# Kernel tuning notes

Hardware: AMD Instinct MI355X
Metric: run time of the kernel (lower is better)

Reference implementation:

```python
import jax, jax.numpy as jnp
import numpy as np

EMBED_DIM = 1024
NUM_HEADS = 16
HEAD_DIM = EMBED_DIM // NUM_HEADS
B, S = 2, 2048


def _xavier(k, shape):
    # xavier_uniform for square [out,in] weight
    limit = float(np.sqrt(6.0 / (shape[0] + shape[1])))
    return jax.random.uniform(k, shape, jnp.float32, -limit, limit)


def setup_inputs() -> dict:
    key = jax.random.key(0)
    ks = jax.random.split(key, 7)
    return {
        "query": jax.random.normal(ks[0], (B, S, EMBED_DIM), jnp.float32),
        "key": jax.random.normal(ks[1], (B, S, EMBED_DIM), jnp.float32),
        "value": jax.random.normal(ks[2], (B, S, EMBED_DIM), jnp.float32),
        "Wq": _xavier(ks[3], (EMBED_DIM, EMBED_DIM)),
        "Wk": _xavier(ks[4], (EMBED_DIM, EMBED_DIM)),
        "Wv": _xavier(ks[5], (EMBED_DIM, EMBED_DIM)),
        "Wo": _xavier(ks[6], (EMBED_DIM, EMBED_DIM)),
    }


def _orthogonalize(Wq, Wk):
    # Both projections computed from the ORIGINAL weights, then both replaced
    # (matches torch: weight1_proj/weight2_proj computed before copy_).
    Wq_o = Wq - Wq @ (Wk.T @ Wk)
    Wk_o = Wk - Wk @ (Wq.T @ Wq)
    return Wq_o, Wk_o


def reference(query, key, value, Wq, Wk, Wv, Wo):
    Wq_o, Wk_o = _orthogonalize(Wq, Wk)
    # F.linear(x, W) = x @ W.T
    q = query @ Wq_o.T
    k = key @ Wk_o.T
    v = value @ Wv.T
    # [B, S, E] -> [B, H, S, Dh]
    def split_heads(x):
        return x.reshape(B, -1, NUM_HEADS, HEAD_DIM).transpose(0, 2, 1, 3)
    q, k, v = split_heads(q), split_heads(k), split_heads(v)
    scale = 1.0 / (HEAD_DIM ** 0.5)
    scores = jnp.einsum("bhqd,bhkd->bhqk", q, k) * scale
    attn = jax.nn.softmax(scores, axis=-1)
    out = jnp.einsum("bhqk,bhkd->bhqd", attn, v)
    out = out.transpose(0, 2, 1, 3).reshape(B, -1, EMBED_DIM)
    return out @ Wo.T
```

## Files before the change

### kernel.cpp

```cpp
#include <hip/hip_runtime.h>
#include <math.h>

constexpr int EMBED  = 1024;
constexpr int NHEADS = 16;
constexpr int HDIM   = 64;
constexpr int BATCH  = 2;
constexpr int SEQ    = 2048;
constexpr int MROWS  = BATCH * SEQ;

typedef unsigned short u16b;
typedef __attribute__((ext_vector_type(8))) short bfrag;
typedef __attribute__((ext_vector_type(4))) float ffrag;

#define SCALE_Q 0.18033688f

__device__ __forceinline__ u16b f2b(float f) {
    union { float f; unsigned u; } v; v.f = f;
    unsigned r = v.u + 0x7fffu + ((v.u >> 16) & 1u);
    return (u16b)(r >> 16);
}
__device__ __forceinline__ u16b f2b_fast(float f) {
    union { float f; unsigned u; } v; v.f = f;
    return (u16b)((v.u + 0x8000u) >> 16);
}

__device__ __forceinline__ void gload_lds16(const u16b* g, u16b* l) {
    __builtin_amdgcn_global_load_lds(
        (const __attribute__((address_space(1))) void*)g,
        (__attribute__((address_space(3))) void*)l,
        16, 0, 0);
}

struct GemmPtrs {
    const u16b* A[3];
    const u16b* B[3];
    const float* D[3];
    u16b* Cb[3];
    float* Cf[3];
    float scale[3];
    int vt[3];
    int hs[3];
};

__global__ void prep_all(const float* __restrict__ q, const float* __restrict__ k,
                         const float* __restrict__ v,
                         const float* __restrict__ Wq, const float* __restrict__ Wk,
                         const float* __restrict__ Wv, const float* __restrict__ Wo,
                         u16b* __restrict__ oq, u16b* __restrict__ ok, u16b* __restrict__ ov,
                         u16b* __restrict__ wq, u16b* __restrict__ wk,
                         u16b* __restrict__ wv, u16b* __restrict__ wo,
                         u16b* __restrict__ wqt, u16b* __restrict__ wkt) {
    const int z = blockIdx.z;
    const int tid = threadIdx.x;
    if (z < 3) {
        const float* src = (z == 0) ? q : (z == 1) ? k : v;
        u16b* dst = (z == 0) ? oq : (z == 1) ? ok : ov;
        const int i = blockIdx.x * 256 + tid;
        float4 val = ((const float4*)src)[i];
        ushort4 o;
        o.x = f2b(val.x); o.y = f2b(val.y); o.z = f2b(val.z); o.w = f2b(val.w);
        ((ushort4*)dst)[i] = o;
        return;
    }
    if (blockIdx.x >= 1024) return;
    const int w = z - 3;
    const float* src = (w == 0) ? Wq : (w == 1) ? Wk : (w == 2) ? Wv : Wo;
    u16b* dst  = (w == 0) ? wq : (w == 1) ? wk : (w == 2) ? wv : wo;
    u16b* dstT = (w == 0) ? wqt : (w == 1) ? wkt : nullptr;
    __shared__ float t[32][33];
    const int bx = (blockIdx.x & 31) * 32, by = (blockIdx.x >> 5) * 32;
    const int x = tid & 31, y = tid >> 5;
#pragma unroll
    for (int r = 0; r < 4; ++r) {
        const int row = by + y + 8 * r;
        const float val = src[(size_t)row * EMBED + bx + x];
        dst[(size_t)row * EMBED + bx + x] = f2b(val);
        if (w < 2) t[y + 8 * r][x] = val;
    }
    if (w >= 2) return;
    __syncthreads();
#pragma unroll
    for (int r = 0; r < 4; ++r)
        dstT[(size_t)(bx + y + 8 * r) * EMBED + by + x] = f2b(t[x][y + 8 * r]);
}

template<int MODE>
__global__ __launch_bounds__(256) void gemm64(GemmPtrs p, int M, int N, int K) {
    const int z = blockIdx.z;
    const u16b* __restrict__ A = p.A[z];
    const u16b* __restrict__ B = p.B[z];
    const float* __restrict__ D = p.D[z];
    u16b* __restrict__ Cb = p.Cb[z];
    const float scale = p.scale[z];

    __shared__ __align__(16) u16b As[64 * 32];
    __shared__ __align__(16) u16b Bs[64 * 32];

    const int tid = threadIdx.x;
    const int wave = tid >> 6, lane = tid & 63;
    const int quad = lane >> 4, l16 = lane & 15;
    const int wrow = wave >> 1, wcol = wave & 1;
    const int m0 = blockIdx.y * 64, n0 = blockIdx.x * 64;

    ffrag acc[2][2];
#pragma unroll
    for (int i = 0; i < 2; ++i)
#pragma unroll
        for (int j = 0; j < 2; ++j) acc[i][j] = ffrag{0.f, 0.f, 0.f, 0.f};

    const int srow = tid >> 2, schunk = tid & 3;

    for (int kt = 0; kt < K; kt += 32) {
        gload_lds16(A + (size_t)(m0 + srow) * K + kt + schunk * 8, &As[wave * 512]);
        gload_lds16(B + (size_t)(n0 + srow) * K + kt + schunk * 8, &Bs[wave * 512]);
        __syncthreads();
        bfrag a[2], bv[2];
#pragma unroll
        for (int i = 0; i < 2; ++i)
            a[i] = *(const bfrag*)&As[(wrow * 32 + i * 16 + l16) * 32 + quad * 8];
#pragma unroll
        for (int j = 0; j < 2; ++j)
            bv[j] = *(const bfrag*)&Bs[(wcol * 32 + j * 16 + l16) * 32 + quad * 8];
#pragma unroll
        for (int i = 0; i < 2; ++i)
#pragma unroll
            for (int j = 0; j < 2; ++j)
                acc[i][j] = __builtin_amdgcn_mfma_f32_16x16x32_bf16(a[i], bv[j], acc[i][j], 0, 0, 0);
        __syncthreads();
    }

#pragma unroll
    for (int i = 0; i < 2; ++i)
#pragma unroll
        for (int j = 0; j < 2; ++j) {
            const int col = n0 + wcol * 32 + j * 16 + l16;
#pragma unroll
            for (int r = 0; r < 4; ++r) {
                const int row = m0 + wrow * 32 + i * 16 + quad * 4 + r;
                const size_t idx = (size_t)row * N + col;
                const float v = acc[i][j][r];
                if (MODE == 0) Cb[idx] = f2b(v * scale);
                else Cb[idx] = f2b(D[idx] - v);
            }
        }
}

template<int MODE, int BM>
__global__ __launch_bounds__(256) void gemm_big(GemmPtrs p, int M, int N, int K) {
    const int z = blockIdx.z;
    const u16b* __restrict__ A = p.A[z];
    const u16b* __restrict__ B = p.B[z];
    u16b* __restrict__ Cb = p.Cb[z];
    float* __restrict__ Cf = p.Cf[z];
    const float scale = p.scale[z];
    const int vt = p.vt[z], hs = p.hs[z];

    constexpr int BK = 32;
    constexpr int IT = BM / 32;
    constexpr int IA = BM / 64;
    __shared__ __align__(16) u16b As[BM * BK];
    __shared__ __align__(16) u16b Bs[128 * BK];

    const int tid = threadIdx.x;
    const int wave = tid >> 6, lane = tid & 63;
    const int quad = lane >> 4, l16 = lane & 15;
    const int wrow = wave >> 1, wcol = wave & 1;
    const int m0 = blockIdx.y * BM, n0 = blockIdx.x * 128;

    ffrag acc[IT][4];
#pragma unroll
    for (int i = 0; i < IT; ++i)
#pragma unroll
        for (int j = 0; j < 4; ++j) acc[i][j] = ffrag{0.f, 0.f, 0.f, 0.f};

    const int srow = lane >> 2, schunk = lane & 3;

    for (int kt = 0; kt < K; kt += BK) {
#pragma unroll
        for (int q = 0; q < IA; ++q) {
            int row = wave * (BM / 4) + q * 16;
            gload_lds16(A + (size_t)(m0 + row + srow) * K + kt + schunk * 8, &As[row * BK]);
        }
#pragma unroll
        for (int q = 0; q < 2; ++q) {
            int row = wave * 32 + q * 16;
            gload_lds16(B + (size_t)(n0 + row + srow) * K + kt + schunk * 8, &Bs[row * BK]);
        }
        __syncthreads();
        bfrag af[IT], bfv[4];
#pragma unroll
        for (int i = 0; i < IT; ++i)
            af[i] = *(const bfrag*)&As[(wrow * (BM / 2) + i * 16 + l16) * BK + quad * 8];
#pragma unroll
        for (int j = 0; j < 4; ++j)
            bfv[j] = *(const bfrag*)&Bs[(wcol * 64 + j * 16 + l16) * BK + quad * 8];
#pragma unroll
        for (int i = 0; i < IT; ++i)
#pragma unroll
            for (int j = 0; j < 4; ++j)
                acc[i][j] = __builtin_amdgcn_mfma_f32_16x16x32_bf16(af[i], bfv[j], acc[i][j], 0, 0, 0);
        __syncthreads();
    }

    if (MODE == 0 && vt) {
#pragma unroll
        for (int i = 0; i < IT; ++i)
#pragma unroll
            for (int j = 0; j < 4; ++j) {
                const int col = n0 + wcol * 64 + j * 16 + l16;
                const int h = col >> 6, d = col & 63;
                const int row0 = m0 + wrow * (BM / 2) + i * 16 + quad * 4;
                const int b = row0 >> 11, s = row0 & 2047;
                ushort4 o;
                o.x = f2b(acc[i][j][0]); o.y = f2b(acc[i][j][1]);
                o.z = f2b(acc[i][j][2]); o.w = f2b(acc[i][j][3]);
                *(ushort4*)&Cb[((size_t)(b * NHEADS + h) * HDIM + d) * SEQ + s] = o;
            }
        return;
    }
    if (MODE == 0 && hs) {
#pragma unroll
        for (int i = 0; i < IT; ++i)
#pragma unroll
            for (int j = 0; j < 4; ++j) {
                const int col = n0 + wcol * 64 + j * 16 + l16;
                const int h = col >> 6, d = col & 63;
                const int row0 = m0 + wrow * (BM / 2) + i * 16 + quad * 4;
                const int b = row0 >> 11, s0 = row0 & 2047;
#pragma unroll
                for (int r = 0; r < 4; ++r)
                    Cb[((size_t)(b * NHEADS + h) * SEQ + s0 + r) * HDIM + d] =
                        f2b(acc[i][j][r] * scale);
            }
        return;
    }

#pragma unroll
    for (int i = 0; i < IT; ++i)
#pragma unroll
        for (int j = 0; j < 4; ++j) {
            const int col = n0 + wcol * 64 + j * 16 + l16;
#pragma unroll
            for (int r = 0; r < 4; ++r) {
                const int row = m0 + wrow * (BM / 2) + i * 16 + quad * 4 + r;
                const size_t idx = (size_t)row * N + col;
                const float v = acc[i][j][r];
                if (MODE == 0) Cb[idx] = f2b(v * scale);
                else Cf[idx] = v;
            }
        }
}

__global__ __launch_bounds__(256) void flash_attn5(
    const u16b* __restrict__ Qp, const u16b* __restrict__ Kp,
    const u16b* __restrict__ Vt, float* __restrict__ Opart,
    float* __restrict__ Lpart)
{
    const int tid = threadIdx.x;
    const int wave = tid >> 6, lane = tid & 63;
    const int quad = lane >> 4, l16 = lane & 15;
    const int qt = blockIdx.x, h = blockIdx.y;
    const int b = blockIdx.z >> 1, sp = blockIdx.z & 1;
    const int qb = qt * 128 + wave * 32;
    const int kt0 = sp * (SEQ / 2), kt1 = kt0 + SEQ / 2;

    __shared__ __align__(16) u16b Ks[2][64 * 64];
    __shared__ __align__(16) u16b Vs[2][64 * 64];
    __shared__ __align__(16) u16b Ps[4][2][16][72];

    const size_t hsbase = (size_t)(b * NHEADS + h) * SEQ;
    const size_t vtbase = (size_t)(b * NHEADS + h) * HDIM * SEQ;
    const size_t obase  = ((size_t)sp * MROWS + (size_t)b * SEQ) * EMBED + h * HDIM;

    bfrag bq[2][2];
#pragma unroll
    for (int u = 0; u < 2; ++u)
#pragma unroll
        for (int s = 0; s < 2; ++s)
            bq[u][s] = *(const bfrag*)&Qp[(hsbase + qb + u * 16 + l16) * HDIM + s * 32 + quad * 8];

    ffrag ov[2][4];
#pragma unroll
    for (int u = 0; u < 2; ++u)
#pragma unroll
        for (int t = 0; t < 4; ++t) ov[u][t] = ffrag{0.f, 0.f, 0.f, 0.f};
    float l_run[2] = {0.f, 0.f};

    const int r0 = tid >> 3, c0 = tid & 7;
    const int sw0 = (r0 * 8 + (c0 ^ (r0 & 7))) * 8;
    const int sw1 = ((r0 + 32) * 8 + (c0 ^ (r0 & 7))) * 8;
    const u16b* kgb = Kp + hsbase * HDIM;
    const u16b* vgb = Vt + vtbase;

    {
        const u16b* kg = kgb + (size_t)kt0 * HDIM;
        bfrag k0 = *(const bfrag*)(kg + tid * 8);
        bfrag k1 = *(const bfrag*)(kg + (tid + 256) * 8);
        bfrag v0 = *(const bfrag*)(vgb + (size_t)r0 * SEQ + kt0 + c0 * 8);
        bfrag v1 = *(const bfrag*)(vgb + (size_t)(r0 + 32) * SEQ + kt0 + c0 * 8);
        *(bfrag*)&Ks[0][sw0] = k0;  *(bfrag*)&Ks[0][sw1] = k1;
        *(bfrag*)&Vs[0][sw0] = v0;  *(bfrag*)&Vs[0][sw1] = v1;
    }
    __syncthreads();

    int p = 0;
    for (int kt = kt0; kt < kt1; kt += 64, p ^= 1) {
        const bool more = (kt + 64) < kt1;
        bfrag kn0, kn1, vn0, vn1;
        if (more) {
            const u16b* kg = kgb + (size_t)(kt + 64) * HDIM;
            kn0 = *(const bfrag*)(kg + tid * 8);
            kn1 = *(const bfrag*)(kg + (tid + 256) * 8);
            vn0 = *(const bfrag*)(vgb + (size_t)r0 * SEQ + kt + 64 + c0 * 8);
            vn1 = *(const bfrag*)(vgb + (size_t)(r0 + 32) * SEQ + kt + 64 + c0 * 8);
        }

        ffrag St[2][4];
#pragma unroll
        for (int u = 0; u < 2; ++u)
#pragma unroll
            for (int t = 0; t < 4; ++t) St[u][t] = ffrag{0.f, 0.f, 0.f, 0.f};
#pragma unroll
        for (int t = 0; t < 4; ++t) {
            const int row = t * 16 + l16;
#pragma unroll
            for (int s = 0; s < 2; ++s) {
                const int ch = quad + s * 4;
                bfrag kf = *(const bfrag*)&Ks[p][(row * 8 + (ch ^ (row & 7))) * 8];
#pragma unroll
                for (int u = 0; u < 2; ++u)
                    St[u][t] = __builtin_amdgcn_mfma_f32_16x16x32_bf16(kf, bq[u][s], St[u][t], 0, 0, 0);
            }
        }

#pragma unroll
        for (int u = 0; u < 2; ++u) {
            float rs = 0.f;
#pragma unroll
            for (int t = 0; t < 4; ++t)
#pragma unroll
                for (int r = 0; r < 4; ++r) {
                    const float pv = __builtin_amdgcn_exp2f(St[u][t][r]);
                    St[u][t][r] = pv;
                    rs += pv;
                }
            rs += __shfl_xor(rs, 16);
            rs += __shfl_xor(rs, 32);
            l_run[u] += rs;
        }

#pragma unroll
        for (int u = 0; u < 2; ++u)
#pragma unroll
            for (int t = 0; t < 4; ++t) {
                ushort4 pk;
                pk.x = f2b_fast(St[u][t][0]); pk.y = f2b_fast(St[u][t][1]);
                pk.z = f2b_fast(St[u][t][2]); pk.w = f2b_fast(St[u][t][3]);
                *(ushort4*)&Ps[wave][u][l16][t * 16 + quad * 4] = pk;
            }
        asm volatile("s_waitcnt lgkmcnt(0)" ::: "memory");
        bfrag bp[2][2];
#pragma unroll
        for (int u = 0; u < 2; ++u)
#pragma unroll
            for (int s = 0; s < 2; ++s)
                bp[u][s] = *(const bfrag*)&Ps[wave][u][l16][s * 32 + quad * 8];

#pragma unroll
        for (int t = 0; t < 4; ++t) {
            const int row = t * 16 + l16;
#pragma unroll
            for (int s = 0; s < 2; ++s) {
                const int ch = quad + s * 4;
                bfrag vf = *(const bfrag*)&Vs[p][(row * 8 + (ch ^ (row & 7))) * 8];
#pragma unroll
                for (int u = 0; u < 2; ++u)
                    ov[u][t] = __builtin_amdgcn_mfma_f32_16x16x32_bf16(vf, bp[u][s], ov[u][t], 0, 0, 0);
            }
        }

        if (more) {
            *(bfrag*)&Ks[p ^ 1][sw0] = kn0;  *(bfrag*)&Ks[p ^ 1][sw1] = kn1;
            *(bfrag*)&Vs[p ^ 1][sw0] = vn0;  *(bfrag*)&Vs[p ^ 1][sw1] = vn1;
            __syncthreads();
        }
    }

#pragma unroll
    for (int u = 0; u < 2; ++u) {
#pragma unroll
        for (int t = 0; t < 4; ++t) {
            float4 o;
            o.x = ov[u][t][0]; o.y = ov[u][t][1];
            o.z = ov[u][t][2]; o.w = ov[u][t][3];
            *(float4*)&Opart[obase + (size_t)(qb + u * 16 + l16) * EMBED + t * 16 + quad * 4] = o;
        }
        if (quad == 0)
            Lpart[((size_t)sp * BATCH * NHEADS + b * NHEADS + h) * SEQ + qb + u * 16 + l16] = l_run[u];
    }
}

__global__ void combine_o(const float* __restrict__ O0, const float* __restrict__ O1,
                          const float* __restrict__ L0, const float* __restrict__ L1,
                          u16b* __restrict__ ao) {
    const int i = blockIdx.x * 256 + threadIdx.x;
    const int e0 = i << 2;
    const int row = e0 >> 10, col = e0 & 1023;
    const int lidx = ((row >> 11) * NHEADS + (col >> 6)) * SEQ + (row & 2047);
    float4 a = ((const float4*)O0)[i];
    float4 c = ((const float4*)O1)[i];
    const float inv = 1.f / (L0[lidx] + L1[lidx]);
    ushort4 o;
    o.x = f2b((a.x + c.x) * inv); o.y = f2b((a.y + c.y) * inv);
    o.z = f2b((a.z + c.z) * inv); o.w = f2b((a.w + c.w) * inv);
    ((ushort4*)ao)[i] = o;
}

extern "C" void kernel_launch(void* const* d_in, const int* in_sizes, int n_in,
                              void* d_out, int out_size, void* d_ws, size_t ws_size,
                              hipStream_t stream) {
    const float* query = (const float*)d_in[0];
    const float* key_  = (const float*)d_in[1];
    const float* value = (const float*)d_in[2];
    const float* Wq    = (const float*)d_in[3];
    const float* Wk    = (const float*)d_in[4];
    const float* Wv    = (const float*)d_in[5];
    const float* Wo    = (const float*)d_in[6];
    float* out = (float*)d_out;

    char* ws = (char*)d_ws;
    const size_t MB = 1024 * 1024;
    u16b* xq  = (u16b*)(ws + 0 * MB);
    u16b* xk  = (u16b*)(ws + 8 * MB);
    u16b* xv  = (u16b*)(ws + 16 * MB);
    u16b* wq  = (u16b*)(ws + 24 * MB);
    u16b* wk  = (u16b*)(ws + 26 * MB);
    u16b* wv  = (u16b*)(ws + 28 * MB);
    u16b* gq  = (u16b*)(ws + 32 * MB);
    u16b* gk  = (u16b*)(ws + 34 * MB);
    u16b* wqo = (u16b*)(ws + 36 * MB);
    u16b* wko = (u16b*)(ws + 38 * MB);
    u16b* wo  = (u16b*)(ws + 40 * MB);
    u16b* qp  = (u16b*)(ws + 44 * MB);
    u16b* kp  = (u16b*)(ws + 52 * MB);
    u16b* Vt  = (u16b*)(ws + 60 * MB);
    u16b* wqt = (u16b*)(ws + 60 * MB);
    u16b* wkt = (u16b*)(ws + 62 * MB);
    float* Op  = (float*)(ws + 0 * MB);
    float* Lp  = (float*)(ws + 32 * MB);
    u16b*  ao  = (u16b*)(ws + 44 * MB);

    prep_all<<<dim3(MROWS * EMBED / 1024, 1, 7), dim3(256), 0, stream>>>(
        query, key_, value, Wq, Wk, Wv, Wo,
        xq, xk, xv, wq, wk, wv, wo, wqt, wkt);

    {
        GemmPtrs p{};
        p.A[0] = wqt; p.B[0] = wqt; p.Cb[0] = gq; p.scale[0] = 1.f;
        p.A[1] = wkt; p.B[1] = wkt; p.Cb[1] = gk; p.scale[1] = 1.f;
        gemm64<0><<<dim3(16, 16, 2), dim3(256), 0, stream>>>(p, EMBED, EMBED, EMBED);
    }
    {
        GemmPtrs p{};
        p.A[0] = wq; p.B[0] = gk; p.D[0] = Wq; p.Cb[0] = wqo;
        p.A[1] = wk; p.B[1] = gq; p.D[1] = Wk; p.Cb[1] = wko;
        gemm64<1><<<dim3(16, 16, 2), dim3(256), 0, stream>>>(p, EMBED, EMBED, EMBED);
    }
    {
        GemmPtrs p{};
        p.A[0] = xq; p.B[0] = wqo; p.Cb[0] = qp; p.scale[0] = SCALE_Q; p.hs[0] = 1;
        p.A[1] = xk; p.B[1] = wko; p.Cb[1] = kp; p.scale[1] = 1.f;     p.hs[1] = 1;
        p.A[2] = xv; p.B[2] = wv;  p.Cb[2] = Vt; p.scale[2] = 1.f;     p.vt[2] = 1;
        gemm_big<0, 128><<<dim3(EMBED / 128, MROWS / 128, 3), dim3(256), 0, stream>>>(
            p, MROWS, EMBED, EMBED);
    }
    flash_attn5<<<dim3(SEQ / 128, NHEADS, BATCH * 2), dim3(256), 0, stream>>>(
        qp, kp, Vt, Op, Lp);
    combine_o<<<dim3(MROWS * EMBED / 1024), dim3(256), 0, stream>>>(
        Op, Op + (size_t)MROWS * EMBED, Lp, Lp + (size_t)BATCH * NHEADS * SEQ, ao);
    {
        GemmPtrs p{};
        p.A[0] = ao; p.B[0] = wo; p.Cf[0] = out; p.scale[0] = 1.f;
        gemm_big<2, 64><<<dim3(EMBED / 128, MROWS / 64, 1), dim3(256), 0, stream>>>(
            p, MROWS, EMBED, EMBED);
    }
}
```

Measured before the change: 294.9 us.

## Use 32x32x16 MFMA in attention and keep P in registers via permlane swaps

Result: no change. 293.3 us (-0.5%).

```diff
diff --git a/kernel.cpp b/kernel.cpp
--- a/kernel.cpp
+++ b/kernel.cpp
@@ -11,6 +11,8 @@
 typedef unsigned short u16b;
 typedef __attribute__((ext_vector_type(8))) short bfrag;
 typedef __attribute__((ext_vector_type(4))) float ffrag;
+typedef __attribute__((ext_vector_type(16))) float f16frag;
+typedef __attribute__((ext_vector_type(4))) int i32x4;
 
 #define SCALE_Q 0.18033688f
 
@@ -19,9 +21,17 @@
     unsigned r = v.u + 0x7fffu + ((v.u >> 16) & 1u);
     return (u16b)(r >> 16);
 }
-__device__ __forceinline__ u16b f2b_fast(float f) {
-    union { float f; unsigned u; } v; v.f = f;
-    return (u16b)((v.u + 0x8000u) >> 16);
+
+__device__ __forceinline__ unsigned cvtpk_bf16(float a, float b) {
+    unsigned r;
+    asm("v_cvt_pk_bf16_f32 %0, %1, %2" : "=v"(r) : "v"(a), "v"(b));
+    return r;
+}
+
+__device__ __forceinline__ void plane_swap(unsigned a, unsigned b, int& lo, int& hi) {
+    auto r = __builtin_amdgcn_permlane32_swap((int)a, (int)b, false, false);
+    lo = (int)r[0];
+    hi = (int)r[1];
 }
 
 __device__ __forceinline__ void gload_lds16(const u16b* g, u16b* l) {
@@ -251,14 +261,14 @@
         }
 }
 
-__global__ __launch_bounds__(256) void flash_attn5(
+__global__ __launch_bounds__(256) void flash_attn6(
     const u16b* __restrict__ Qp, const u16b* __restrict__ Kp,
     const u16b* __restrict__ Vt, float* __restrict__ Opart,
     float* __restrict__ Lpart)
 {
     const int tid = threadIdx.x;
     const int wave = tid >> 6, lane = tid & 63;
-    const int quad = lane >> 4, l16 = lane & 15;
+    const int l32 = lane & 31, hi = lane >> 5;
     const int qt = blockIdx.x, h = blockIdx.y;
     const int b = blockIdx.z >> 1, sp = blockIdx.z & 1;
     const int qb = qt * 128 + wave * 32;
@@ -266,25 +276,20 @@
 
     __shared__ __align__(16) u16b Ks[2][64 * 64];
     __shared__ __align__(16) u16b Vs[2][64 * 64];
-    __shared__ __align__(16) u16b Ps[4][2][16][72];
 
     const size_t hsbase = (size_t)(b * NHEADS + h) * SEQ;
     const size_t vtbase = (size_t)(b * NHEADS + h) * HDIM * SEQ;
     const size_t obase  = ((size_t)sp * MROWS + (size_t)b * SEQ) * EMBED + h * HDIM;
 
-    bfrag bq[2][2];
-#pragma unroll
-    for (int u = 0; u < 2; ++u)
-#pragma unroll
-        for (int s = 0; s < 2; ++s)
-            bq[u][s] = *(const bfrag*)&Qp[(hsbase + qb + u * 16 + l16) * HDIM + s * 32 + quad * 8];
-
-    ffrag ov[2][4];
-#pragma unroll
-    for (int u = 0; u < 2; ++u)
-#pragma unroll
-        for (int t = 0; t < 4; ++t) ov[u][t] = ffrag{0.f, 0.f, 0.f, 0.f};
-    float l_run[2] = {0.f, 0.f};
+    bfrag bq[4];
+#pragma unroll
+    for (int ks = 0; ks < 4; ++ks)
+        bq[ks] = *(const bfrag*)&Qp[(hsbase + qb + l32) * HDIM + ks * 16 + hi * 8];
+
+    f16frag ov0, ov1;
+#pragma unroll
+    for (int r = 0; r < 16; ++r) { ov0[r] = 0.f; ov1[r] = 0.f; }
+    float l_run = 0.f;
 
     const int r0 = tid >> 3, c0 = tid & 7;
     const int sw0 = (r0 * 8 + (c0 ^ (r0 & 7))) * 8;
@@ -315,68 +320,66 @@
             vn1 = *(const bfrag*)(vgb + (size_t)(r0 + 32) * SEQ + kt + 64 + c0 * 8);
         }
 
-        ffrag St[2][4];
-#pragma unroll
-        for (int u = 0; u < 2; ++u)
-#pragma unroll
-            for (int t = 0; t < 4; ++t) St[u][t] = ffrag{0.f, 0.f, 0.f, 0.f};
-#pragma unroll
-        for (int t = 0; t < 4; ++t) {
-            const int row = t * 16 + l16;
-#pragma unroll
-            for (int s = 0; s < 2; ++s) {
-                const int ch = quad + s * 4;
-                bfrag kf = *(const bfrag*)&Ks[p][(row * 8 + (ch ^ (row & 7))) * 8];
-#pragma unroll
-                for (int u = 0; u < 2; ++u)
-                    St[u][t] = __builtin_amdgcn_mfma_f32_16x16x32_bf16(kf, bq[u][s], St[u][t], 0, 0, 0);
-            }
-        }
-
-#pragma unroll
-        for (int u = 0; u < 2; ++u) {
-            float rs = 0.f;
-#pragma unroll
-            for (int t = 0; t < 4; ++t)
-#pragma unroll
-                for (int r = 0; r < 4; ++r) {
-                    const float pv = __builtin_amdgcn_exp2f(St[u][t][r]);
-                    St[u][t][r] = pv;
-                    rs += pv;
-                }
-            rs += __shfl_xor(rs, 16);
-            rs += __shfl_xor(rs, 32);
-            l_run[u] += rs;
-        }
-
-#pragma unroll
-        for (int u = 0; u < 2; ++u)
-#pragma unroll
-            for (int t = 0; t < 4; ++t) {
-                ushort4 pk;
-                pk.x = f2b_fast(St[u][t][0]); pk.y = f2b_fast(St[u][t][1]);
-                pk.z = f2b_fast(St[u][t][2]); pk.w = f2b_fast(St[u][t][3]);
-                *(ushort4*)&Ps[wave][u][l16][t * 16 + quad * 4] = pk;
-            }
-        asm volatile("s_waitcnt lgkmcnt(0)" ::: "memory");
-        bfrag bp[2][2];
-#pragma unroll
-        for (int u = 0; u < 2; ++u)
-#pragma unroll
-            for (int s = 0; s < 2; ++s)
-                bp[u][s] = *(const bfrag*)&Ps[wave][u][l16][s * 32 + quad * 8];
-
-#pragma unroll
-        for (int t = 0; t < 4; ++t) {
-            const int row = t * 16 + l16;
-#pragma unroll
-            for (int s = 0; s < 2; ++s) {
-                const int ch = quad + s * 4;
-                bfrag vf = *(const bfrag*)&Vs[p][(row * 8 + (ch ^ (row & 7))) * 8];
-#pragma unroll
-                for (int u = 0; u < 2; ++u)
-                    ov[u][t] = __builtin_amdgcn_mfma_f32_16x16x32_bf16(vf, bp[u][s], ov[u][t], 0, 0, 0);
-            }
+        f16frag St0, St1;
+#pragma unroll
+        for (int r = 0; r < 16; ++r) { St0[r] = 0.f; St1[r] = 0.f; }
+#pragma unroll
+        for (int ks = 0; ks < 4; ++ks) {
+            const int ch = ks * 2 + hi;
+            bfrag k0 = *(const bfrag*)&Ks[p][(l32 * 8 + (ch ^ (l32 & 7))) * 8];
+            bfrag k1 = *(const bfrag*)&Ks[p][((32 + l32) * 8 + (ch ^ (l32 & 7))) * 8];
+            St0 = __builtin_amdgcn_mfma_f32_32x32x16_bf16(k0, bq[ks], St0, 0, 0, 0);
+            St1 = __builtin_amdgcn_mfma_f32_32x32x16_bf16(k1, bq[ks], St1, 0, 0, 0);
+        }
+
+        float rs = 0.f;
+#pragma unroll
+        for (int r = 0; r < 16; ++r) {
+            const float a = __builtin_amdgcn_exp2f(St0[r]);
+            const float c = __builtin_amdgcn_exp2f(St1[r]);
+            St0[r] = a; St1[r] = c;
+            rs += a + c;
+        }
+        rs += __shfl_xor(rs, 32);
+        l_run += rs;
+
+        unsigned d0[8], d1[8];
+#pragma unroll
+        for (int rr = 0; rr < 8; ++rr) {
+            d0[rr] = cvtpk_bf16(St0[2 * rr], St0[2 * rr + 1]);
+            d1[rr] = cvtpk_bf16(St1[2 * rr], St1[2 * rr + 1]);
+        }
+        bfrag bp[4];
+        {
+            int a0, a1, b0, b1, c0w, c1, e0, e1;
+            plane_swap(d0[0], d0[2], a0, a1);
+            plane_swap(d0[1], d0[3], b0, b1);
+            i32x4 w = { a0, b0, a1, b1 };
+            bp[0] = __builtin_bit_cast(bfrag, w);
+            plane_swap(d0[4], d0[6], c0w, c1);
+            plane_swap(d0[5], d0[7], e0, e1);
+            i32x4 w2 = { c0w, e0, c1, e1 };
+            bp[1] = __builtin_bit_cast(bfrag, w2);
+        }
+        {
+            int a0, a1, b0, b1, c0w, c1, e0, e1;
+            plane_swap(d1[0], d1[2], a0, a1);
+            plane_swap(d1[1], d1[3], b0, b1);
+            i32x4 w = { a0, b0, a1, b1 };
+            bp[2] = __builtin_bit_cast(bfrag, w);
+            plane_swap(d1[4], d1[6], c0w, c1);
+            plane_swap(d1[5], d1[7], e0, e1);
+            i32x4 w2 = { c0w, e0, c1, e1 };
+            bp[3] = __builtin_bit_cast(bfrag, w2);
+        }
+
+#pragma unroll
+        for (int ks = 0; ks < 4; ++ks) {
+            const int ch = ks * 2 + hi;
+            bfrag v0 = *(const bfrag*)&Vs[p][(l32 * 8 + (ch ^ (l32 & 7))) * 8];
+            bfrag v1 = *(const bfrag*)&Vs[p][((32 + l32) * 8 + (ch ^ (l32 & 7))) * 8];
+            ov0 = __builtin_amdgcn_mfma_f32_32x32x16_bf16(v0, bp[ks], ov0, 0, 0, 0);
+            ov1 = __builtin_amdgcn_mfma_f32_32x32x16_bf16(v1, bp[ks], ov1, 0, 0, 0);
         }
 
         if (more) {
@@ -386,18 +389,19 @@
         }
     }
 
-#pragma unroll
-    for (int u = 0; u < 2; ++u) {
-#pragma unroll
-        for (int t = 0; t < 4; ++t) {
-            float4 o;
-            o.x = ov[u][t][0]; o.y = ov[u][t][1];
-            o.z = ov[u][t][2]; o.w = ov[u][t][3];
-            *(float4*)&Opart[obase + (size_t)(qb + u * 16 + l16) * EMBED + t * 16 + quad * 4] = o;
-        }
-        if (quad == 0)
-            Lpart[((size_t)sp * BATCH * NHEADS + b * NHEADS + h) * SEQ + qb + u * 16 + l16] = l_run[u];
-    }
+    const size_t orow = obase + (size_t)(qb + l32) * EMBED;
+#pragma unroll
+    for (int rr = 0; rr < 4; ++rr) {
+        float4 o0, o1;
+        o0.x = ov0[4 * rr + 0]; o0.y = ov0[4 * rr + 1];
+        o0.z = ov0[4 * rr + 2]; o0.w = ov0[4 * rr + 3];
+        o1.x = ov1[4 * rr + 0]; o1.y = ov1[4 * rr + 1];
+        o1.z = ov1[4 * rr + 2]; o1.w = ov1[4 * rr + 3];
+        *(float4*)&Opart[orow + rr * 8 + hi * 4] = o0;
+        *(float4*)&Opart[orow + 32 + rr * 8 + hi * 4] = o1;
+    }
+    if (hi == 0)
+        Lpart[((size_t)sp * BATCH * NHEADS + b * NHEADS + h) * SEQ + qb + l32] = l_run;
 }
 
 __global__ void combine_o(const float* __restrict__ O0, const float* __restrict__ O1,
@@ -474,7 +478,7 @@
         gemm_big<0, 128><<<dim3(EMBED / 128, MROWS / 128, 3), dim3(256), 0, stream>>>(
             p, MROWS, EMBED, EMBED);
     }
-    flash_attn5<<<dim3(SEQ / 128, NHEADS, BATCH * 2), dim3(256), 0, stream>>>(
+    flash_attn6<<<dim3(SEQ / 128, NHEADS, BATCH * 2), dim3(256), 0, stream>>>(
         qp, kp, Vt, Op, Lp);
     combine_o<<<dim3(MROWS * EMBED / 1024), dim3(256), 0, stream>>>(
         Op, Op + (size_t)MROWS * EMBED, Lp, Lp + (size_t)BATCH * NHEADS * SEQ, ao);
```
